# Performance work log

Measured on AMD Instinct MI355X. Metric: run time of the kernel, lower is better.

## Reference

```python
import jax, jax.numpy as jnp
import numpy as np

N_NODES = 100000
N_EDGES = 1600000
IN_FEAT = 64
OUT_FEAT = 64


def setup_inputs() -> dict:
    key = jax.random.key(0)
    k_h, k_src, k_dst, k_w, k_b = jax.random.split(key, 5)
    h = jax.random.normal(k_h, (N_NODES, IN_FEAT), dtype=jnp.float32)
    src = jax.random.randint(k_src, (N_EDGES,), 0, N_NODES, dtype=jnp.int64)
    dst = jax.random.randint(k_dst, (N_EDGES,), 0, N_NODES, dtype=jnp.int64)
    # nn.Linear(in_feat*2, out_feat): weight [out, 2*in], bias [out]
    W = jax.random.normal(k_w, (OUT_FEAT, 2 * IN_FEAT), dtype=jnp.float32) * 0.05
    b = jax.random.normal(k_b, (OUT_FEAT,), dtype=jnp.float32) * 0.05
    return {"h": h, "src": src, "dst": dst, "W": W, "b": b}


def reference(h, src, dst, W, b):
    # message = copy_u: gather source-node features along edges  [E, F]
    msgs = h[src]
    # mean reduce per destination node (DGL mean -> 0 for isolated nodes)
    summed = jax.ops.segment_sum(msgs, dst, num_segments=N_NODES)  # [N, F]
    deg = jax.ops.segment_sum(jnp.ones((src.shape[0],), dtype=h.dtype), dst,
                              num_segments=N_NODES)                # [N]
    h_N = summed / jnp.maximum(deg, 1.0)[:, None]
    h_total = jnp.concatenate([h, h_N], axis=1)                    # [N, 2F]
    return h_total @ W.T + b
```

## Files before the change

### kernel.cpp

```cpp
#include <hip/hip_runtime.h>

#define IN_FEAT 64
#define OUT_FEAT 64
#define CAP 48
#define NB 196
#define BUFCAP 64
#define QPAD 16
#define ROUTE_BLOCKS 512

typedef __attribute__((ext_vector_type(8))) _Float16 half8;
typedef __attribute__((ext_vector_type(4))) float floatx4;
typedef __attribute__((ext_vector_type(4))) int intx4;

__global__ __launch_bounds__(512) void route_kernel(const int* __restrict__ src,
        const int* __restrict__ dst, int* __restrict__ qtail,
        int* __restrict__ queue, int E, int qcap, int epb,
        const float* __restrict__ h, _Float16* __restrict__ h16, int total8) {
    for (int t = blockIdx.x * 512 + threadIdx.x; t < total8;
         t += ROUTE_BLOCKS * 512) {
        const float4* p = (const float4*)(h + (long long)t * 8);
        float4 a = p[0], c = p[1];
        half8 v;
        v[0] = (_Float16)a.x; v[1] = (_Float16)a.y;
        v[2] = (_Float16)a.z; v[3] = (_Float16)a.w;
        v[4] = (_Float16)c.x; v[5] = (_Float16)c.y;
        v[6] = (_Float16)c.z; v[7] = (_Float16)c.w;
        *(half8*)(h16 + (long long)t * 8) = v;
    }

    __shared__ int cnt[NB];
    __shared__ int sbase[NB];
    __shared__ __align__(16) int buf[NB * BUFCAP];
    int tid = threadIdx.x;
    int eb = blockIdx.x * epb;
    int ee = eb + epb; if (ee > E) ee = E;
    for (int r0 = eb; r0 < ee; r0 += 512 * 8) {
        for (int i = tid; i < NB; i += 512) cnt[i] = 0;
        __syncthreads();
#pragma unroll
        for (int k = 0; k < 8; ++k) {
            int e = r0 + k * 512 + tid;
            if (e < ee) {
                int d = dst[e];
                int s = src[e];
                int b = d >> 9;
                int entry = ((d & 511) << 17) | s;
                int pos = atomicAdd(&cnt[b], 1);
                if (pos < BUFCAP) buf[b * BUFCAP + pos] = entry;
                else {
                    int p2 = atomicAdd(&qtail[b * QPAD], 1);
                    if (p2 < qcap) queue[(long long)b * qcap + p2] = entry;
                }
            }
        }
        __syncthreads();
        if (tid < NB) {
            int n = cnt[tid]; if (n > BUFCAP) n = BUFCAP;
            sbase[tid] = (n > 0) ? atomicAdd(&qtail[tid * QPAD], n) : 0;
        }
        __syncthreads();
        int w = tid >> 6, lane = tid & 63;
        int b1 = w * 25 + 25; if (b1 > NB) b1 = NB;
        for (int b = w * 25; b < b1; ++b) {
            int n = cnt[b]; if (n > BUFCAP) n = BUFCAP;
            if (lane < n) {
                int p = sbase[b] + lane;
                if (p < qcap) queue[(long long)b * qcap + p] = buf[b * BUFCAP + lane];
            }
        }
        __syncthreads();
    }
}

__global__ __launch_bounds__(512, 1) void build_kernel(const int* __restrict__ qtail,
        const int* __restrict__ queue, int* __restrict__ deg,
        int* __restrict__ csr, int N, int qcap) {
    __shared__ __align__(16) int lcsr[512 * CAP];
    __shared__ int ldeg[512];
    int tid = threadIdx.x;
    int bid = blockIdx.x;
    if (tid < 512) ldeg[tid] = 0;
    __syncthreads();
    int qn = qtail[bid * QPAD]; if (qn > qcap) qn = qcap;
    long long qb = (long long)bid * qcap;
    for (int i = tid; i < qn; i += 512) {
        int e = queue[qb + i];
        int dl = e >> 17;
        int s = e & 0x1FFFF;
        int pos = atomicAdd(&ldeg[dl], 1);
        if (pos < CAP) lcsr[dl * CAP + pos] = s;
    }
    __syncthreads();
    int base_node = bid << 9;
    int nn = N - base_node; if (nn > 512) nn = 512;
    if (nn <= 0) return;
    for (int i4 = tid; i4 < nn * (CAP / 4); i4 += 512) {
        int r = i4 / (CAP / 4), c4 = i4 % (CAP / 4);
        intx4 v = *(intx4*)&lcsr[r * CAP + c4 * 4];
        *(intx4*)&csr[((long long)(base_node + r) << 6) + c4 * 4] = v;
    }
    for (int i = tid; i < nn; i += 512) deg[base_node + i] = ldeg[i];
}

__global__ __launch_bounds__(256) void gather_kernel(const _Float16* __restrict__ h16,
        const int* __restrict__ deg, int* csr_x, int N) {
    int wave = threadIdx.x >> 6;
    int lane = threadIdx.x & 63;
    int n0 = (blockIdx.x * 4 + wave) * 4;
    if (n0 >= N) return;
#pragma unroll
    for (int it = 0; it < 2; ++it) {
        int a = n0 + it * 2;
        if (a >= N) return;
        int bn = a + 1;
        bool hasB = bn < N;
        int cntA = deg[a];
        int cntB = hasB ? deg[bn] : 0;
        int rawA = csr_x[(a << 6) | lane];
        int rawB = hasB ? csr_x[(bn << 6) | lane] : 0;
        _Float16 selfA = h16[(long long)a * IN_FEAT + lane];
        _Float16 selfB = hasB ? h16[(long long)bn * IN_FEAT + lane] : (_Float16)0.0f;
        int mA = cntA < CAP ? cntA : CAP;
        int mB = cntB < CAP ? cntB : CAP;
        int sidA = (lane < mA) ? rawA : 0;
        int sidB = (lane < mB) ? rawB : 0;
        float accA0 = 0.f, accA1 = 0.f, accB0 = 0.f, accB1 = 0.f;
        int mmax = mA > mB ? mA : mB;
        for (int j = 0; j < mmax; j += 8) {
            float va[8], vb[8];
#pragma unroll
            for (int k = 0; k < 8; ++k) {
                int sA = __shfl(sidA, j + k);
                int sB = __shfl(sidB, j + k);
                va[k] = (float)h16[(long long)sA * IN_FEAT + lane];
                vb[k] = (float)h16[(long long)sB * IN_FEAT + lane];
            }
#pragma unroll
            for (int k = 0; k < 8; ++k) {
                float xa = (j + k < mA) ? va[k] : 0.0f;
                float xb = (j + k < mB) ? vb[k] : 0.0f;
                if (k & 1) { accA1 += xa; accB1 += xb; }
                else       { accA0 += xa; accB0 += xb; }
            }
        }
        float meanA = (accA0 + accA1) / fmaxf((float)cntA, 1.0f);
        _Float16* xrA = (_Float16*)(csr_x + ((long long)a << 6));
        xrA[lane] = selfA;
        xrA[IN_FEAT + lane] = (_Float16)meanA;
        if (hasB) {
            float meanB = (accB0 + accB1) / fmaxf((float)cntB, 1.0f);
            _Float16* xrB = (_Float16*)(csr_x + ((long long)bn << 6));
            xrB[lane] = selfB;
            xrB[IN_FEAT + lane] = (_Float16)meanB;
        }
    }
}

__global__ __launch_bounds__(256) void linear_kernel(const int* __restrict__ x_i,
        const float* __restrict__ W, const float* __restrict__ b,
        float* __restrict__ out, int N) {
    const _Float16* x = (const _Float16*)x_i;
    __shared__ _Float16 wlds[16 * 64 * 8];
    int wave = threadIdx.x >> 6;
    int lane = threadIdx.x & 63;
    int quad = lane >> 4;
    int l16  = lane & 15;
    for (int i = threadIdx.x; i < 64 * 2 * IN_FEAT; i += 256) {
        int row = i >> 7, col = i & 127;
        int t = row >> 4, lr = row & 15;
        int q = col >> 5, qd = (col & 31) >> 3, j = col & 7;
        wlds[(((t * 4 + q) * 64) + (qd * 16 + lr)) * 8 + j] = (_Float16)W[i];
    }
    __syncthreads();
    int node_base = (blockIdx.x * 4 + wave) * 16;
    if (node_base >= N) return;
    half8 bf[4][4];
#pragma unroll
    for (int t = 0; t < 4; ++t)
#pragma unroll
        for (int q = 0; q < 4; ++q)
            bf[t][q] = *(const half8*)&wlds[((t * 4 + q) * 64 + lane) * 8];
    float bias[4];
#pragma unroll
    for (int t = 0; t < 4; ++t) bias[t] = b[16 * t + l16];
    int mrow = node_base + l16;
    if (mrow >= N) mrow = N - 1;
    floatx4 z = {0.0f, 0.0f, 0.0f, 0.0f};
    floatx4 acc[4] = {z, z, z, z};
#pragma unroll
    for (int q = 0; q < 4; ++q) {
        half8 af = *(const half8*)&x[(long long)mrow * (2 * IN_FEAT) + 32 * q + 8 * quad];
#pragma unroll
        for (int t = 0; t < 4; ++t)
            acc[t] = __builtin_amdgcn_mfma_f32_16x16x32_f16(af, bf[t][q], acc[t], 0, 0, 0);
    }
#pragma unroll
    for (int t = 0; t < 4; ++t)
#pragma unroll
        for (int r = 0; r < 4; ++r) {
            int n = node_base + quad * 4 + r;
            if (n < N)
                out[(long long)n * OUT_FEAT + 16 * t + l16] = acc[t][r] + bias[t];
        }
}

extern "C" void kernel_launch(void* const* d_in, const int* in_sizes, int n_in,
                              void* d_out, int out_size, void* d_ws, size_t ws_size,
                              hipStream_t stream) {
    const float* h   = (const float*)d_in[0];
    const int*   src = (const int*)d_in[1];
    const int*   dst = (const int*)d_in[2];
    const float* W   = (const float*)d_in[3];
    const float* b   = (const float*)d_in[4];
    float* out = (float*)d_out;

    int N = in_sizes[0] / IN_FEAT;
    int E = in_sizes[1];

    int qcap = (int)((long long)E * 512 / N) + 1024;
    int epb  = (E + ROUTE_BLOCKS - 1) / ROUTE_BLOCKS;
    int nbr  = (N + 511) >> 9;

    int* deg   = (int*)d_ws;
    int* csr   = deg + N;
    int* qtail = csr + (size_t)N * 64;
    int* queue = qtail + NB * QPAD;
    _Float16* h16 = (_Float16*)out;

    int total8 = N * IN_FEAT / 8;
    (void)hipMemsetAsync(qtail, 0, (size_t)NB * QPAD * sizeof(int), stream);
    route_kernel<<<ROUTE_BLOCKS, 512, 0, stream>>>(src, dst, qtail, queue,
                                                   E, qcap, epb, h, h16, total8);
    build_kernel<<<nbr, 512, 0, stream>>>(qtail, queue, deg, csr, N, qcap);

    gather_kernel<<<(N + 15) / 16, 256, 0, stream>>>(h16, deg, csr, N);

    int tiles = (N + 15) / 16;
    linear_kernel<<<(tiles + 3) / 4, 256, 0, stream>>>(csr, W, b, out, N);
}
```

Before: 166.4 us.

## Fuse CSR build with neighbor gather using 256-node buckets in LDS

Merges the build and gather kernels so each block builds its local adjacency list in shared memory and immediately aggregates neighbor features from it. This removes the global CSR and degree round trip and one kernel launch. Buckets shrink to 256 nodes (392 buckets, 32-entry staging buffers) so the per-block LDS adjacency fits and more blocks can be resident. Only 8 waves per block now do the gather over 256 nodes, which may reduce latency hiding compared with the previous separate, finer-grained gather launch.

```diff
diff --git a/kernel.cpp b/kernel.cpp
--- a/kernel.cpp
+++ b/kernel.cpp
@@ -3,8 +3,8 @@
 #define IN_FEAT 64
 #define OUT_FEAT 64
 #define CAP 48
-#define NB 196
-#define BUFCAP 64
+#define NB 392
+#define BUFCAP 32
 #define QPAD 16
 #define ROUTE_BLOCKS 512
 
@@ -43,8 +43,8 @@
             if (e < ee) {
                 int d = dst[e];
                 int s = src[e];
-                int b = d >> 9;
-                int entry = ((d & 511) << 17) | s;
+                int b = d >> 8;
+                int entry = ((d & 255) << 17) | s;
                 int pos = atomicAdd(&cnt[b], 1);
                 if (pos < BUFCAP) buf[b * BUFCAP + pos] = entry;
                 else {
@@ -60,8 +60,8 @@
         }
         __syncthreads();
         int w = tid >> 6, lane = tid & 63;
-        int b1 = w * 25 + 25; if (b1 > NB) b1 = NB;
-        for (int b = w * 25; b < b1; ++b) {
+        int b0 = w * 49, b1 = b0 + 49; if (b1 > NB) b1 = NB;
+        for (int b = b0; b < b1; ++b) {
             int n = cnt[b]; if (n > BUFCAP) n = BUFCAP;
             if (lane < n) {
                 int p = sbase[b] + lane;
@@ -72,14 +72,15 @@
     }
 }
 
-__global__ __launch_bounds__(512, 1) void build_kernel(const int* __restrict__ qtail,
-        const int* __restrict__ queue, int* __restrict__ deg,
-        int* __restrict__ csr, int N, int qcap) {
-    __shared__ __align__(16) int lcsr[512 * CAP];
-    __shared__ int ldeg[512];
+__global__ __launch_bounds__(512) void buildgather_kernel(
+        const int* __restrict__ qtail, const int* __restrict__ queue,
+        const _Float16* __restrict__ h16, int* __restrict__ x_i,
+        int N, int qcap) {
+    __shared__ __align__(16) int lcsr[256 * CAP];
+    __shared__ int ldeg[256];
     int tid = threadIdx.x;
     int bid = blockIdx.x;
-    if (tid < 512) ldeg[tid] = 0;
+    if (tid < 256) ldeg[tid] = 0;
     __syncthreads();
     int qn = qtail[bid * QPAD]; if (qn > qcap) qn = qcap;
     long long qb = (long long)bid * qcap;
@@ -91,39 +92,24 @@
         if (pos < CAP) lcsr[dl * CAP + pos] = s;
     }
     __syncthreads();
-    int base_node = bid << 9;
-    int nn = N - base_node; if (nn > 512) nn = 512;
-    if (nn <= 0) return;
-    for (int i4 = tid; i4 < nn * (CAP / 4); i4 += 512) {
-        int r = i4 / (CAP / 4), c4 = i4 % (CAP / 4);
-        intx4 v = *(intx4*)&lcsr[r * CAP + c4 * 4];
-        *(intx4*)&csr[((long long)(base_node + r) << 6) + c4 * 4] = v;
-    }
-    for (int i = tid; i < nn; i += 512) deg[base_node + i] = ldeg[i];
-}
-
-__global__ __launch_bounds__(256) void gather_kernel(const _Float16* __restrict__ h16,
-        const int* __restrict__ deg, int* csr_x, int N) {
-    int wave = threadIdx.x >> 6;
-    int lane = threadIdx.x & 63;
-    int n0 = (blockIdx.x * 4 + wave) * 4;
-    if (n0 >= N) return;
-#pragma unroll
-    for (int it = 0; it < 2; ++it) {
-        int a = n0 + it * 2;
-        if (a >= N) return;
+
+    int base = bid << 8;
+    int wave = tid >> 6, lane = tid & 63;
+#pragma unroll 1
+    for (int it = 0; it < 16; ++it) {
+        int a = base + wave * 32 + it * 2;
+        if (a >= N) break;
         int bn = a + 1;
-        bool hasB = bn < N;
-        int cntA = deg[a];
-        int cntB = hasB ? deg[bn] : 0;
-        int rawA = csr_x[(a << 6) | lane];
-        int rawB = hasB ? csr_x[(bn << 6) | lane] : 0;
-        _Float16 selfA = h16[(long long)a * IN_FEAT + lane];
-        _Float16 selfB = hasB ? h16[(long long)bn * IN_FEAT + lane] : (_Float16)0.0f;
+        bool okB = bn < N;
+        int la = a - base, lb = la + 1;
+        int cntA = ldeg[la];
+        int cntB = okB ? ldeg[lb] : 0;
         int mA = cntA < CAP ? cntA : CAP;
         int mB = cntB < CAP ? cntB : CAP;
-        int sidA = (lane < mA) ? rawA : 0;
-        int sidB = (lane < mB) ? rawB : 0;
+        int sidA = (lane < mA) ? lcsr[la * CAP + lane] : 0;
+        int sidB = (okB && lane < mB) ? lcsr[lb * CAP + lane] : 0;
+        _Float16 selfA = h16[(long long)a * IN_FEAT + lane];
+        _Float16 selfB = okB ? h16[(long long)bn * IN_FEAT + lane] : (_Float16)0.0f;
         float accA0 = 0.f, accA1 = 0.f, accB0 = 0.f, accB1 = 0.f;
         int mmax = mA > mB ? mA : mB;
         for (int j = 0; j < mmax; j += 8) {
@@ -144,12 +130,12 @@
             }
         }
         float meanA = (accA0 + accA1) / fmaxf((float)cntA, 1.0f);
-        _Float16* xrA = (_Float16*)(csr_x + ((long long)a << 6));
+        _Float16* xrA = (_Float16*)(x_i + ((long long)a << 6));
         xrA[lane] = selfA;
         xrA[IN_FEAT + lane] = (_Float16)meanA;
-        if (hasB) {
+        if (okB) {
             float meanB = (accB0 + accB1) / fmaxf((float)cntB, 1.0f);
-            _Float16* xrB = (_Float16*)(csr_x + ((long long)bn << 6));
+            _Float16* xrB = (_Float16*)(x_i + ((long long)bn << 6));
             xrB[lane] = selfB;
             xrB[IN_FEAT + lane] = (_Float16)meanB;
         }
@@ -217,13 +203,12 @@
     int N = in_sizes[0] / IN_FEAT;
     int E = in_sizes[1];
 
-    int qcap = (int)((long long)E * 512 / N) + 1024;
+    int qcap = (int)((long long)E * 256 / N) + 768;
     int epb  = (E + ROUTE_BLOCKS - 1) / ROUTE_BLOCKS;
-    int nbr  = (N + 511) >> 9;
-
-    int* deg   = (int*)d_ws;
-    int* csr   = deg + N;
-    int* qtail = csr + (size_t)N * 64;
+    int nbr  = (N + 255) >> 8;
+
+    int* x_i   = (int*)d_ws;
+    int* qtail = x_i + (size_t)N * 64;
     int* queue = qtail + NB * QPAD;
     _Float16* h16 = (_Float16*)out;
 
@@ -231,10 +216,8 @@
     (void)hipMemsetAsync(qtail, 0, (size_t)NB * QPAD * sizeof(int), stream);
     route_kernel<<<ROUTE_BLOCKS, 512, 0, stream>>>(src, dst, qtail, queue,
                                                    E, qcap, epb, h, h16, total8);
-    build_kernel<<<nbr, 512, 0, stream>>>(qtail, queue, deg, csr, N, qcap);
-
-    gather_kernel<<<(N + 15) / 16, 256, 0, stream>>>(h16, deg, csr, N);
+    buildgather_kernel<<<nbr, 512, 0, stream>>>(qtail, queue, h16, x_i, N, qcap);
 
     int tiles = (N + 15) / 16;
-    linear_kernel<<<(tiles + 3) / 4, 256, 0, stream>>>(csr, W, b, out, N);
-}
+    linear_kernel<<<(tiles + 3) / 4, 256, 0, stream>>>(x_i, W, b, out, N);
+}
```

Measured after the change: 181.4 us. 1.09x slower.
